# Kernel optimization log

Measured on AMD Instinct MI355X. Metric: run time of the kernel, lower is better.

## Reference

```python
import jax, jax.numpy as jnp
import numpy as np

ENC, PRED, H, V, DMAX = 1024, 640, 640, 1024, 4
B, T, U = 4, 256, 64


def setup_inputs() -> dict:
    key = jax.random.key(0)
    ks = jax.random.split(key, 10)
    s = lambda d: 1.0 / np.sqrt(d)
    return {
        "encoder_out": jax.random.normal(ks[0], (B, T, ENC), jnp.float32),
        "predictor_out": jax.random.normal(ks[1], (B, U, PRED), jnp.float32),
        "W_enc": jax.random.uniform(ks[2], (H, ENC), jnp.float32, -s(ENC), s(ENC)),
        "b_enc": jax.random.uniform(ks[3], (H,), jnp.float32, -s(ENC), s(ENC)),
        "W_pred": jax.random.uniform(ks[4], (H, PRED), jnp.float32, -s(PRED), s(PRED)),
        "b_pred": jax.random.uniform(ks[5], (H,), jnp.float32, -s(PRED), s(PRED)),
        "W_out": jax.random.uniform(ks[6], (V, H), jnp.float32, -s(H), s(H)),
        "b_out": jax.random.uniform(ks[7], (V,), jnp.float32, -s(H), s(H)),
        "W_dur": jax.random.uniform(ks[8], (DMAX + 1, H), jnp.float32, -s(H), s(H)),
        "b_dur": jax.random.uniform(ks[9], (DMAX + 1,), jnp.float32, -s(H), s(H)),
    }


def reference(encoder_out, predictor_out, W_enc, b_enc, W_pred, b_pred,
              W_out, b_out, W_dur, b_dur):
    # Project encoder [B,T,H] and predictor [B,U,H]
    enc = jnp.einsum('bte,he->bth', encoder_out, W_enc) + b_enc
    pred = jnp.einsum('bup,hp->buh', predictor_out, W_pred) + b_pred
    # Broadcast-add -> [B,T,U,H], tanh
    joint = jnp.tanh(enc[:, :, None, :] + pred[:, None, :, :])
    # Dual heads
    logits = jnp.einsum('btuh,vh->btuv', joint, W_out) + b_out        # [B,T,U,V]
    durations = jnp.einsum('btuh,dh->btud', joint, W_dur) + b_dur     # [B,T,U,DMAX+1]
    return (logits, durations)
```

## Files before the change

kernel.cpp:

```cpp
#include <hip/hip_runtime.h>

typedef unsigned short u16;
typedef unsigned int u32;

typedef __bf16 bf16x8 __attribute__((ext_vector_type(8)));
typedef float f32x4 __attribute__((ext_vector_type(4)));

union FragI { int4 i; bf16x8 b; };
union FragU { bf16x8 b; u16 u[8]; };

__device__ __forceinline__ u16 f2bf(float x) {
  u32 u = __float_as_uint(x);
  u32 r = (u + 0x7fffu + ((u >> 16) & 1u)) >> 16;
  return (u16)r;
}

__device__ __forceinline__ float tanh_fast(float x) {
  float e = __expf(2.0f * x);
  return 1.0f - __fdividef(2.0f, e + 1.0f);
}

__device__ __forceinline__ bf16x8 load_cvt8(const float* __restrict__ p) {
  float4 f0 = *(const float4*)p;
  float4 f1 = *(const float4*)(p + 4);
  FragU t;
  t.u[0] = f2bf(f0.x); t.u[1] = f2bf(f0.y); t.u[2] = f2bf(f0.z); t.u[3] = f2bf(f0.w);
  t.u[4] = f2bf(f1.x); t.u[5] = f2bf(f1.y); t.u[6] = f2bf(f1.z); t.u[7] = f2bf(f1.w);
  return t.b;
}

#define GLDS(gptr, lptr) \
  __builtin_amdgcn_global_load_lds((const __attribute__((address_space(1))) u32*)(gptr), \
                                   (__attribute__((address_space(3))) u32*)(lptr), 16, 0, 0)

__global__ __launch_bounds__(256) void conv_v4(const float* __restrict__ in,
                                               u16* __restrict__ out, int n4) {
  int i = blockIdx.x * 256 + threadIdx.x;
  if (i >= n4) return;
  float4 f = ((const float4*)in)[i];
  union { u16 u[4]; int2 v; } o;
  o.u[0] = f2bf(f.x); o.u[1] = f2bf(f.y); o.u[2] = f2bf(f.z); o.u[3] = f2bf(f.w);
  ((int2*)out)[i] = o.v;
}

__global__ __launch_bounds__(256) void conv_wdur(const float* __restrict__ in,
                                                 u16* __restrict__ out) {
  int i = blockIdx.x * 256 + threadIdx.x;
  if (i < 16 * 640) out[i] = (i < 5 * 640) ? f2bf(in[i]) : (u16)0;
}

__global__ __launch_bounds__(256) void proj_gemm(const float* __restrict__ A,
                                                 const float* __restrict__ Bw,
                                                 const float* __restrict__ bias,
                                                 float* __restrict__ C,
                                                 int M, int N, int K) {
  int tid = threadIdx.x;
  int lane = tid & 63, wid = tid >> 6;
  int m0 = blockIdx.x * 64, n0 = blockIdx.y * 64;
  int kper = K >> 2;
  int kbase = wid * kper;
  int ksteps = kper >> 5;
  int r16 = lane & 15, khi = (lane >> 4) * 8;

  f32x4 z = {0.f, 0.f, 0.f, 0.f};
  f32x4 acc[4][4];
  for (int i = 0; i < 4; ++i)
    for (int j = 0; j < 4; ++j) acc[i][j] = z;

  for (int ks = 0; ks < ksteps; ++ks) {
    int k = kbase + ks * 32 + khi;
    bf16x8 af[4], bf[4];
#pragma unroll
    for (int fm = 0; fm < 4; ++fm)
      af[fm] = load_cvt8(A + (size_t)(m0 + fm * 16 + r16) * K + k);
#pragma unroll
    for (int fn = 0; fn < 4; ++fn)
      bf[fn] = load_cvt8(Bw + (size_t)(n0 + fn * 16 + r16) * K + k);
#pragma unroll
    for (int fm = 0; fm < 4; ++fm)
#pragma unroll
      for (int fn = 0; fn < 4; ++fn)
        acc[fm][fn] = __builtin_amdgcn_mfma_f32_16x16x32_bf16(af[fm], bf[fn], acc[fm][fn], 0, 0, 0);
  }

  __shared__ float red[4][64][64];
#pragma unroll
  for (int fm = 0; fm < 4; ++fm)
#pragma unroll
    for (int fn = 0; fn < 4; ++fn)
#pragma unroll
      for (int i = 0; i < 4; ++i)
        red[wid][fm * 16 + (lane >> 4) * 4 + i][fn * 16 + r16] = acc[fm][fn][i];
  __syncthreads();
  for (int idx = tid; idx < 4096; idx += 256) {
    int r = idx >> 6, c = idx & 63;
    float s = red[0][r][c] + red[1][r][c] + red[2][r][c] + red[3][r][c] + bias[n0 + c];
    C[(size_t)(m0 + r) * N + n0 + c] = s;
  }
}

__global__ __launch_bounds__(256) void joint_tanh(const float* __restrict__ enc,
                                                  const float* __restrict__ pred,
                                                  u16* __restrict__ J) {
  const int total = 65536 * 80;
  for (int c = blockIdx.x * 256 + threadIdx.x; c < total; c += gridDim.x * 256) {
    int m = c / 80;
    int j = c - m * 80;
    int bt = m >> 6;
    int uu = m & 63;
    int b = bt >> 8;
    const float* ep = enc + bt * 640 + j * 8;
    const float* pp = pred + (b * 64 + uu) * 640 + j * 8;
    float4 e0 = *(const float4*)ep;
    float4 e1 = *(const float4*)(ep + 4);
    float4 p0 = *(const float4*)pp;
    float4 p1 = *(const float4*)(pp + 4);
    union { u16 u[8]; int4 v; } o;
    o.u[0] = f2bf(tanh_fast(e0.x + p0.x));
    o.u[1] = f2bf(tanh_fast(e0.y + p0.y));
    o.u[2] = f2bf(tanh_fast(e0.z + p0.z));
    o.u[3] = f2bf(tanh_fast(e0.w + p0.w));
    o.u[4] = f2bf(tanh_fast(e1.x + p1.x));
    o.u[5] = f2bf(tanh_fast(e1.y + p1.y));
    o.u[6] = f2bf(tanh_fast(e1.z + p1.z));
    o.u[7] = f2bf(tanh_fast(e1.w + p1.w));
    *(int4*)(J + (size_t)c * 8) = o.v;
  }
}

#define LOGITS_N 67108864

__device__ __forceinline__ void stage128(const u16* __restrict__ g, u16* l,
                                         int wid, int lane) {
  int rl = wid * 8 + (lane >> 3);
  int cl = ((lane & 7) ^ (lane >> 3)) * 8;
  const u16* gp = g + (size_t)rl * 640 + cl;
  u16* lp = l + wid * 512;
#pragma unroll
  for (int j = 0; j < 4; ++j)
    GLDS(gp + (size_t)j * 32 * 640, lp + j * 2048);
}

__global__ __launch_bounds__(256, 2) void main_gemm(const u16* __restrict__ J,
                                                    const u16* __restrict__ Wo,
                                                    const u16* __restrict__ Wd,
                                                    const float* __restrict__ b_out,
                                                    const float* __restrict__ b_dur,
                                                    float* __restrict__ out) {
  __shared__ __align__(16) u16 As[2][8192];
  __shared__ __align__(16) u16 Bs[2][8192];
  int tid = threadIdx.x;
  int lane = tid & 63, wid = tid >> 6;
  int bid = blockIdx.x;
  int swz = (bid & 7) * 512 + (bid >> 3);
  int bn = swz & 7, bm = swz >> 3;
  int m0 = bm * 128, n0 = bn * 128;
  int wr = wid >> 1, wc = wid & 1;
  int r16 = lane & 15, khi = (lane >> 4) * 8;
  int xorv = (r16 & 7) << 3;
  bool do_dur = (bn == 0);

  f32x4 z = {0.f, 0.f, 0.f, 0.f};
  f32x4 acc[4][4];
#pragma unroll
  for (int i = 0; i < 4; ++i)
#pragma unroll
    for (int j = 0; j < 4; ++j) acc[i][j] = z;
  f32x4 dacc[4] = {z, z, z, z};

  const u16* Jb = J + (size_t)m0 * 640;
  const u16* Wb = Wo + (size_t)n0 * 640;
  stage128(Jb + 0, As[0], wid, lane);
  stage128(Wb + 0, Bs[0], wid, lane);
  stage128(Jb + 64, As[1], wid, lane);
  stage128(Wb + 64, Bs[1], wid, lane);

#pragma unroll
  for (int t = 0; t < 10; ++t) {
    const int p = t & 1;
    if (t < 9) {
      asm volatile("s_waitcnt vmcnt(8)" ::: "memory");
    } else {
      asm volatile("s_waitcnt vmcnt(0)" ::: "memory");
    }
    __builtin_amdgcn_sched_barrier(0);
    __builtin_amdgcn_s_barrier();
    __builtin_amdgcn_sched_barrier(0);
    const u16* Ab = As[p];
    const u16* Bb = Bs[p];
#pragma unroll
    for (int ks = 0; ks < 2; ++ks) {
      int cks = (ks * 32 + khi) ^ xorv;
      FragI af[4], bfr[4], wd;
#pragma unroll
      for (int fn = 0; fn < 4; ++fn)
        bfr[fn].i = *(const int4*)(Bb + (wc * 64 + fn * 16 + r16) * 64 + cks);
#pragma unroll
      for (int fm = 0; fm < 4; ++fm)
        af[fm].i = *(const int4*)(Ab + (wr * 64 + fm * 16 + r16) * 64 + cks);
      if (do_dur)
        wd.i = *(const int4*)(Wd + (size_t)r16 * 640 + t * 64 + ks * 32 + khi);
      __builtin_amdgcn_s_setprio(1);
#pragma unroll
      for (int fm = 0; fm < 4; ++fm) {
#pragma unroll
        for (int fn = 0; fn < 4; ++fn)
          acc[fm][fn] = __builtin_amdgcn_mfma_f32_16x16x32_bf16(af[fm].b, bfr[fn].b, acc[fm][fn], 0, 0, 0);
        if (do_dur)
          dacc[fm] = __builtin_amdgcn_mfma_f32_16x16x32_bf16(af[fm].b, wd.b, dacc[fm], 0, 0, 0);
      }
      __builtin_amdgcn_s_setprio(0);
    }
    if (t < 9) {
      __builtin_amdgcn_sched_barrier(0);
      asm volatile("s_waitcnt lgkmcnt(0)" ::: "memory");
      __builtin_amdgcn_s_barrier();
      __builtin_amdgcn_sched_barrier(0);
      if (t + 2 < 10) {
        stage128(Jb + (t + 2) * 64, As[p], wid, lane);
        stage128(Wb + (t + 2) * 64, Bs[p], wid, lane);
      }
    }
  }

  int rb = m0 + wr * 64 + (lane >> 4) * 4;
  int cb = n0 + wc * 64 + r16;
#pragma unroll
  for (int fn = 0; fn < 4; ++fn) {
    int col = cb + fn * 16;
    float bo = b_out[col];
#pragma unroll
    for (int fm = 0; fm < 4; ++fm) {
      int row = rb + fm * 16;
#pragma unroll
      for (int i = 0; i < 4; ++i)
        out[(size_t)(row + i) * 1024 + col] = acc[fm][fn][i] + bo;
    }
  }
  if (do_dur && r16 < 5) {
    float bd = b_dur[r16];
#pragma unroll
    for (int fm = 0; fm < 4; ++fm) {
      int row = rb + fm * 16;
#pragma unroll
      for (int i = 0; i < 4; ++i)
        out[LOGITS_N + (size_t)(row + i) * 5 + r16] = dacc[fm][i] + bd;
    }
  }
}

extern "C" void kernel_launch(void* const* d_in, const int* in_sizes, int n_in,
                              void* d_out, int out_size, void* d_ws, size_t ws_size,
                              hipStream_t stream) {
  const float* encoder   = (const float*)d_in[0];
  const float* predictor = (const float*)d_in[1];
  const float* W_enc = (const float*)d_in[2];
  const float* b_enc = (const float*)d_in[3];
  const float* W_pred = (const float*)d_in[4];
  const float* b_pred = (const float*)d_in[5];
  const float* W_out = (const float*)d_in[6];
  const float* b_out = (const float*)d_in[7];
  const float* W_dur = (const float*)d_in[8];
  const float* b_dur = (const float*)d_in[9];
  float* out = (float*)d_out;

  char* ws = (char*)d_ws;
  u16* Jbuf    = (u16*)(ws);
  u16* WoutB   = (u16*)(ws + 83886080);
  u16* WdurB   = (u16*)(ws + 85196800);
  float* encP  = (float*)(ws + 85217280);
  float* predP = (float*)(ws + 87838720);

  conv_v4<<<640, 256, 0, stream>>>(W_out, WoutB, 163840);
  conv_wdur<<<40, 256, 0, stream>>>(W_dur, WdurB);
  proj_gemm<<<dim3(16, 10), 256, 0, stream>>>(encoder, W_enc, b_enc, encP, 1024, 640, 1024);
  proj_gemm<<<dim3(4, 10), 256, 0, stream>>>(predictor, W_pred, b_pred, predP, 256, 640, 640);
  joint_tanh<<<2048, 256, 0, stream>>>(encP, predP, Jbuf);
  main_gemm<<<4096, 256, 0, stream>>>(Jbuf, WoutB, WdurB, b_out, b_dur, out);
}
```

Before: 208.2 us.

## Replace LDS-staged double buffering with direct global fragment loads in main GEMM

The main bf16 GEMM no longer stages J and W_out tiles through shared memory with global_load_lds double buffering and barriers. Each wave now loads its MFMA fragments straight from global memory (relying on L1/L2 for reuse) in a plain K loop unrolled by two, and launch bounds raise occupancy to three blocks per CU. This removes LDS traffic, barriers and the waitcnt pipeline, but every wave fetches its operands separately from cache with uncoalesced 16-byte row-strided loads and no explicit prefetch overlap.

```diff
diff --git a/kernel.cpp b/kernel.cpp
--- a/kernel.cpp
+++ b/kernel.cpp
@@ -28,10 +28,6 @@
   t.u[4] = f2bf(f1.x); t.u[5] = f2bf(f1.y); t.u[6] = f2bf(f1.z); t.u[7] = f2bf(f1.w);
   return t.b;
 }
-
-#define GLDS(gptr, lptr) \
-  __builtin_amdgcn_global_load_lds((const __attribute__((address_space(1))) u32*)(gptr), \
-                                   (__attribute__((address_space(3))) u32*)(lptr), 16, 0, 0)
 
 __global__ __launch_bounds__(256) void conv_v4(const float* __restrict__ in,
                                                u16* __restrict__ out, int n4) {
@@ -130,25 +126,12 @@
 
 #define LOGITS_N 67108864
 
-__device__ __forceinline__ void stage128(const u16* __restrict__ g, u16* l,
-                                         int wid, int lane) {
-  int rl = wid * 8 + (lane >> 3);
-  int cl = ((lane & 7) ^ (lane >> 3)) * 8;
-  const u16* gp = g + (size_t)rl * 640 + cl;
-  u16* lp = l + wid * 512;
-#pragma unroll
-  for (int j = 0; j < 4; ++j)
-    GLDS(gp + (size_t)j * 32 * 640, lp + j * 2048);
-}
-
-__global__ __launch_bounds__(256, 2) void main_gemm(const u16* __restrict__ J,
+__global__ __launch_bounds__(256, 3) void main_gemm(const u16* __restrict__ J,
                                                     const u16* __restrict__ Wo,
                                                     const u16* __restrict__ Wd,
                                                     const float* __restrict__ b_out,
                                                     const float* __restrict__ b_dur,
                                                     float* __restrict__ out) {
-  __shared__ __align__(16) u16 As[2][8192];
-  __shared__ __align__(16) u16 Bs[2][8192];
   int tid = threadIdx.x;
   int lane = tid & 63, wid = tid >> 6;
   int bid = blockIdx.x;
@@ -156,9 +139,18 @@
   int bn = swz & 7, bm = swz >> 3;
   int m0 = bm * 128, n0 = bn * 128;
   int wr = wid >> 1, wc = wid & 1;
-  int r16 = lane & 15, khi = (lane >> 4) * 8;
-  int xorv = (r16 & 7) << 3;
+  int r16 = lane & 15, khi8 = (lane >> 4) * 8;
   bool do_dur = (bn == 0);
+
+  const u16* Ap[4];
+  const u16* Bp[4];
+#pragma unroll
+  for (int fm = 0; fm < 4; ++fm)
+    Ap[fm] = J + (size_t)(m0 + wr * 64 + fm * 16 + r16) * 640 + khi8;
+#pragma unroll
+  for (int fn = 0; fn < 4; ++fn)
+    Bp[fn] = Wo + (size_t)(n0 + wc * 64 + fn * 16 + r16) * 640 + khi8;
+  const u16* Wp = Wd + (size_t)r16 * 640 + khi8;
 
   f32x4 z = {0.f, 0.f, 0.f, 0.f};
   f32x4 acc[4][4];
@@ -168,58 +160,24 @@
     for (int j = 0; j < 4; ++j) acc[i][j] = z;
   f32x4 dacc[4] = {z, z, z, z};
 
-  const u16* Jb = J + (size_t)m0 * 640;
-  const u16* Wb = Wo + (size_t)n0 * 640;
-  stage128(Jb + 0, As[0], wid, lane);
-  stage128(Wb + 0, Bs[0], wid, lane);
-  stage128(Jb + 64, As[1], wid, lane);
-  stage128(Wb + 64, Bs[1], wid, lane);
-
-#pragma unroll
-  for (int t = 0; t < 10; ++t) {
-    const int p = t & 1;
-    if (t < 9) {
-      asm volatile("s_waitcnt vmcnt(8)" ::: "memory");
-    } else {
-      asm volatile("s_waitcnt vmcnt(0)" ::: "memory");
-    }
-    __builtin_amdgcn_sched_barrier(0);
-    __builtin_amdgcn_s_barrier();
-    __builtin_amdgcn_sched_barrier(0);
-    const u16* Ab = As[p];
-    const u16* Bb = Bs[p];
-#pragma unroll
-    for (int ks = 0; ks < 2; ++ks) {
-      int cks = (ks * 32 + khi) ^ xorv;
-      FragI af[4], bfr[4], wd;
+#pragma unroll 2
+  for (int kof = 0; kof < 640; kof += 32) {
+    FragI af[4], bfr[4], wd;
+#pragma unroll
+    for (int fm = 0; fm < 4; ++fm)
+      af[fm].i = *(const int4*)(Ap[fm] + kof);
+#pragma unroll
+    for (int fn = 0; fn < 4; ++fn)
+      bfr[fn].i = *(const int4*)(Bp[fn] + kof);
+    if (do_dur)
+      wd.i = *(const int4*)(Wp + kof);
+#pragma unroll
+    for (int fm = 0; fm < 4; ++fm) {
 #pragma unroll
       for (int fn = 0; fn < 4; ++fn)
-        bfr[fn].i = *(const int4*)(Bb + (wc * 64 + fn * 16 + r16) * 64 + cks);
-#pragma unroll
-      for (int fm = 0; fm < 4; ++fm)
-        af[fm].i = *(const int4*)(Ab + (wr * 64 + fm * 16 + r16) * 64 + cks);
+        acc[fm][fn] = __builtin_amdgcn_mfma_f32_16x16x32_bf16(af[fm].b, bfr[fn].b, acc[fm][fn], 0, 0, 0);
       if (do_dur)
-        wd.i = *(const int4*)(Wd + (size_t)r16 * 640 + t * 64 + ks * 32 + khi);
-      __builtin_amdgcn_s_setprio(1);
-#pragma unroll
-      for (int fm = 0; fm < 4; ++fm) {
-#pragma unroll
-        for (int fn = 0; fn < 4; ++fn)
-          acc[fm][fn] = __builtin_amdgcn_mfma_f32_16x16x32_bf16(af[fm].b, bfr[fn].b, acc[fm][fn], 0, 0, 0);
-        if (do_dur)
-          dacc[fm] = __builtin_amdgcn_mfma_f32_16x16x32_bf16(af[fm].b, wd.b, dacc[fm], 0, 0, 0);
-      }
-      __builtin_amdgcn_s_setprio(0);
-    }
-    if (t < 9) {
-      __builtin_amdgcn_sched_barrier(0);
-      asm volatile("s_waitcnt lgkmcnt(0)" ::: "memory");
-      __builtin_amdgcn_s_barrier();
-      __builtin_amdgcn_sched_barrier(0);
-      if (t + 2 < 10) {
-        stage128(Jb + (t + 2) * 64, As[p], wid, lane);
-        stage128(Wb + (t + 2) * 64, Bs[p], wid, lane);
-      }
+        dacc[fm] = __builtin_amdgcn_mfma_f32_16x16x32_bf16(af[fm].b, wd.b, dacc[fm], 0, 0, 0);
     }
   }
 
```

Result: slower. 394.2 us (+89.3%).
